# Optimization experiments

Hardware: AMD Instinct MI355X
Metric: run time of the kernel (lower is better)

## Reference

```python
import jax, jax.numpy as jnp
import numpy as np

M = 0.4        # margin
H = 0.333      # margin scaler slope
S = 64.0       # logit scale
BN_MEAN = 20.0     # running_mean of norm normalizer (affine=False, eval stats)
BN_VAR = 100.0 * 100.0
BN_EPS = 1e-3


def setup_inputs() -> dict:
    key = jax.random.key(0)
    k1, k2, k3 = jax.random.split(key, 3)
    embs = jax.random.normal(k1, (1024, 512), dtype=jnp.float32)
    weight = jax.random.normal(k2, (100000, 512), dtype=jnp.float32)
    labels = jax.random.randint(k3, (1024,), 0, 100000)
    return {"embs": embs, "weight": weight, "labels": labels}


def reference(embs, weight, labels):
    n = embs.shape[0]
    rows = jnp.arange(n)
    # feature norms and cosine logits
    norms = jnp.linalg.norm(embs, axis=1, keepdims=True)            # [N,1]
    w_norm = weight / jnp.linalg.norm(weight, axis=1, keepdims=True)  # [C,D]
    logits = (embs / norms) @ w_norm.T                               # [N,C]
    # norm-adaptive margin scaler (BatchNorm1d with running stats, affine=False)
    g = (norms[:, 0] - BN_MEAN) / jnp.sqrt(BN_VAR + BN_EPS)
    g = jnp.clip(g * H, -1.0, 1.0)                                   # [N]
    # angular margin at the label position
    theta = jnp.arccos(jnp.clip(logits.astype(jnp.float32), -0.999, 0.999))
    theta = theta.at[rows, labels].add(-M * g)
    logits_m = jnp.cos(jnp.clip(theta, 0.0, jnp.pi))
    # additive margin at the label position
    logits_m = logits_m.at[rows, labels].add(-(1.0 + M) * g)
    # scaled softmax cross-entropy (mean over batch)
    logp = jax.nn.log_softmax(logits_m * S, axis=-1)
    return -jnp.mean(logp[rows, labels])
```

## Files before the change

kernel.cpp:

```cpp
#include <hip/hip_runtime.h>
#include <math.h>

constexpr int N_ROWS = 1024;
constexpr int DDIM   = 512;
constexpr int C_CLS  = 100000;
constexpr float MARG = 0.4f;
constexpr int NT8    = 784;
constexpr int WPAD8  = 100352;
constexpr int NT_FB  = 782;

typedef __attribute__((ext_vector_type(8))) short bf16x8;
typedef __attribute__((ext_vector_type(4))) float f32x4;
typedef __attribute__((ext_vector_type(4))) int   i32x4;
typedef __attribute__((ext_vector_type(8))) int   i32x8;
typedef __attribute__((address_space(1))) const void gvoid_t;
typedef __attribute__((address_space(3))) void lvoid_t;

__device__ __forceinline__ unsigned int f2bf(float x) {
    union { float f; unsigned int u; } v; v.f = x;
    return (v.u + 0x7FFFu + ((v.u >> 16) & 1u)) >> 16;
}

__device__ __forceinline__ float wave_sum(float s) {
    #pragma unroll
    for (int m = 1; m < 64; m <<= 1) s += __shfl_xor(s, m, 64);
    return s;
}

#if __has_builtin(__builtin_amdgcn_cvt_pk_fp8_f32)
__device__ __forceinline__ unsigned int pk4_e4m3(float a, float b, float c, float d) {
    unsigned int u = (unsigned int)__builtin_amdgcn_cvt_pk_fp8_f32(a, b, 0, false);
    u = (unsigned int)__builtin_amdgcn_cvt_pk_fp8_f32(c, d, (int)u, true);
    return u;
}
#else
__device__ __forceinline__ unsigned int sw_e4m3(float x) {
    x = fminf(fmaxf(x, -448.f), 448.f);
    unsigned int s = (x < 0.f) ? 0x80u : 0u;
    float ax = fabsf(x);
    if (ax < 7.8125e-3f) {
        int q = (int)rintf(ax * 512.f);
        if (q >= 8) return s | 0x08;
        return s | (unsigned int)q;
    }
    int e; float m = frexpf(ax, &e);
    int q = (int)rintf(m * 16.f);
    if (q == 16) { q = 8; e += 1; }
    int E = e - 1 + 7;
    if (E > 15) { E = 15; q = 14; }
    return s | ((unsigned int)E << 3) | (unsigned int)(q - 8);
}
__device__ __forceinline__ unsigned int pk4_e4m3(float a, float b, float c, float d) {
    return sw_e4m3(a) | (sw_e4m3(b) << 8) | (sw_e4m3(c) << 16) | (sw_e4m3(d) << 24);
}
#endif

__device__ __forceinline__ float dec_e4m3(unsigned int b) {
    const unsigned int E = (b >> 3) & 15u, M = b & 7u;
    if (E) {
        union { unsigned int u; float f; } v;
        v.u = ((b & 0x80u) << 24) | ((E + 120u) << 23) | (M << 20);
        return v.f;
    }
    float d = (float)M * 0.001953125f;
    return (b & 0x80u) ? -d : d;
}

__global__ __launch_bounds__(256) void prep_embs8(const float* __restrict__ embs,
                                                  float* __restrict__ g,
                                                  unsigned char* __restrict__ ehat8) {
    const int row  = blockIdx.x * 4 + (threadIdx.x >> 6);
    const int lane = threadIdx.x & 63;
    const float4* src = (const float4*)(embs + (size_t)row * DDIM + lane * 8);
    const float4 a = src[0], b = src[1];
    float ss = a.x*a.x + a.y*a.y + a.z*a.z + a.w*a.w
             + b.x*b.x + b.y*b.y + b.z*b.z + b.w*b.w;
    ss = wave_sum(ss);
    const float norm = sqrtf(ss);
    const float rn = 1.f / norm;
    if (lane == 0) {
        float gg = (norm - 20.f) / sqrtf(10000.f + 1e-3f) * 0.333f;
        gg = fminf(fmaxf(gg, -1.f), 1.f);
        g[row] = gg;
    }
    uint2 pk;
    pk.x = pk4_e4m3(a.x*rn, a.y*rn, a.z*rn, a.w*rn);
    pk.y = pk4_e4m3(b.x*rn, b.y*rn, b.z*rn, b.w*rn);
    *(uint2*)(ehat8 + (size_t)row * DDIM + lane * 8) = pk;
}

__global__ __launch_bounds__(256) void prep_what8(const float* __restrict__ w,
                                                  unsigned char* __restrict__ what8) {
    const int row  = blockIdx.x * 4 + (threadIdx.x >> 6);
    const int lane = threadIdx.x & 63;
    if (row >= C_CLS) {
        *(uint2*)(what8 + (size_t)row * DDIM + lane * 8) = make_uint2(0u, 0u);
        return;
    }
    const float4* src = (const float4*)(w + (size_t)row * DDIM + lane * 8);
    const float4 a = src[0], b = src[1];
    float ss = a.x*a.x + a.y*a.y + a.z*a.z + a.w*a.w
             + b.x*b.x + b.y*b.y + b.z*b.z + b.w*b.w;
    ss = wave_sum(ss);
    const float rn = rsqrtf(ss);
    uint2 pk;
    pk.x = pk4_e4m3(a.x*rn, a.y*rn, a.z*rn, a.w*rn);
    pk.y = pk4_e4m3(b.x*rn, b.y*rn, b.z*rn, b.w*rn);
    *(uint2*)(what8 + (size_t)row * DDIM + lane * 8) = pk;
}

__device__ __forceinline__ i32x8 join8(i32x4 lo, i32x4 hi) {
    return __builtin_shufflevector(lo, hi, 0, 1, 2, 3, 4, 5, 6, 7);
}

__global__ __launch_bounds__(256, 2) void gemm_s1(
        const unsigned char* __restrict__ ehat8,
        const unsigned char* __restrict__ what8,
        float* __restrict__ psum)
{
    __shared__ __align__(16) unsigned char Ab[16384];
    __shared__ __align__(16) unsigned char Bb[16384];
    __shared__ float redbuf[2][128];

    const int tid  = threadIdx.x;
    const int lane = tid & 63;
    const int wv   = tid >> 6;
    const int wr   = wv >> 1;
    const int wc   = wv & 1;
    const int r    = lane & 15;
    const int q    = lane >> 4;

    const int wgid   = ((int)blockIdx.x & 7) * 784 + ((int)blockIdx.x >> 3);
    const int tile_c = wgid >> 3;
    const int tile_r = wgid & 7;
    const int row0   = tile_r * 128;
    const int col0   = tile_c * 128;

    const unsigned char* Asrc = ehat8 + (size_t)(row0 + r) * DDIM + q * 32;
    const unsigned char* Bsrc = what8 + (size_t)(col0 + r) * DDIM + q * 32;

    f32x4 acc[4][4];
    #pragma unroll
    for (int m = 0; m < 4; ++m)
        #pragma unroll
        for (int n = 0; n < 4; ++n) acc[m][n] = f32x4{0.f, 0.f, 0.f, 0.f};

    const int t0 = (int)blockIdx.x & 3;

    for (int it = 0; it < 4; ++it) {
        const int t = (t0 + it) & 3;
        #pragma unroll
        for (int ss = 0; ss < 2; ++ss) {
            const int sl = wv * 2 + ss;
            const unsigned char* ga = Asrc + (size_t)(16 * sl) * DDIM + t * 128;
            __builtin_amdgcn_global_load_lds((gvoid_t*)ga,        (lvoid_t*)(Ab + sl * 2048),        16, 0, 0);
            __builtin_amdgcn_global_load_lds((gvoid_t*)(ga + 16), (lvoid_t*)(Ab + sl * 2048 + 1024), 16, 0, 0);
            const unsigned char* gb = Bsrc + (size_t)(16 * sl) * DDIM + t * 128;
            __builtin_amdgcn_global_load_lds((gvoid_t*)gb,        (lvoid_t*)(Bb + sl * 2048),        16, 0, 0);
            __builtin_amdgcn_global_load_lds((gvoid_t*)(gb + 16), (lvoid_t*)(Bb + sl * 2048 + 1024), 16, 0, 0);
        }
        __syncthreads();

        i32x4 bR[4][2];
        #pragma unroll
        for (int n = 0; n < 4; ++n) {
            bR[n][0] = *(const i32x4*)(Bb + (wc * 4 + n) * 2048 +        lane * 16);
            bR[n][1] = *(const i32x4*)(Bb + (wc * 4 + n) * 2048 + 1024 + lane * 16);
        }
        __builtin_amdgcn_s_setprio(1);
        #pragma unroll
        for (int m = 0; m < 4; ++m) {
            const i32x4 a0 = *(const i32x4*)(Ab + (wr * 4 + m) * 2048 +        lane * 16);
            const i32x4 a1 = *(const i32x4*)(Ab + (wr * 4 + m) * 2048 + 1024 + lane * 16);
            const i32x8 av = join8(a0, a1);
            #pragma unroll
            for (int n = 0; n < 4; ++n)
                acc[m][n] = __builtin_amdgcn_mfma_scale_f32_16x16x128_f8f6f4(
                                av, join8(bR[n][0], bR[n][1]), acc[m][n], 0, 0, 0, 127, 0, 127);
        }
        __builtin_amdgcn_s_setprio(0);
        __syncthreads();
    }

    #pragma unroll
    for (int m = 0; m < 4; ++m) {
        #pragma unroll
        for (int j = 0; j < 4; ++j) {
            const int lrow = wr * 64 + m * 16 + q * 4 + j;
            float s = 0.f;
            #pragma unroll
            for (int n = 0; n < 4; ++n) {
                float v = acc[m][n][j];
                v = fminf(fmaxf(v, -0.999f), 0.999f);
                s += __expf(64.f * v - 64.f);
            }
            #pragma unroll
            for (int msk = 1; msk < 16; msk <<= 1) s += __shfl_xor(s, msk, 64);
            if (r == 0) redbuf[wc][lrow] = s;
        }
    }
    __syncthreads();
    for (int t = tid; t < 128; t += 256)
        psum[(size_t)(row0 + t) * NT8 + tile_c] = redbuf[0][t] + redbuf[1][t];
}

__global__ __launch_bounds__(256) void reduce_rows8(
        const float* __restrict__ psum,
        const unsigned char* __restrict__ ehat8,
        const unsigned char* __restrict__ what8,
        const int* __restrict__ labels,
        const float* __restrict__ g,
        float* __restrict__ losses) {
    const int row  = blockIdx.x * 4 + (threadIdx.x >> 6);
    const int lane = threadIdx.x & 63;
    const float* p = psum + (size_t)row * NT8;
    float s = 0.f;
    for (int t = lane; t < NT8; t += 64) s += p[t];
    const int lab = labels[row];
    const uint2 ea = *(const uint2*)(ehat8 + (size_t)row * DDIM + lane * 8);
    const uint2 wa = *(const uint2*)(what8 + (size_t)lab * DDIM + lane * 8);
    float d = 0.f;
    #pragma unroll
    for (int i = 0; i < 4; ++i)
        d += dec_e4m3((ea.x >> (8 * i)) & 0xFFu) * dec_e4m3((wa.x >> (8 * i)) & 0xFFu);
    #pragma unroll
    for (int i = 0; i < 4; ++i)
        d += dec_e4m3((ea.y >> (8 * i)) & 0xFFu) * dec_e4m3((wa.y >> (8 * i)) & 0xFFu);
    s = wave_sum(s);
    d = wave_sum(d);
    if (lane == 0) {
        const float v  = fminf(fmaxf(d, -0.999f), 0.999f);
        const float gg = g[row];
        float th = acosf(v) - MARG * gg;
        th = fminf(fmaxf(th, 0.f), 3.14159265358979323846f);
        const float vm = cosf(th) - (1.f + MARG) * gg;
        s = s - __expf(64.f * v - 64.f) + __expf(64.f * vm - 64.f);
        losses[row] = 64.f + logf(s) - 64.f * vm;
    }
}

__global__ __launch_bounds__(256) void prep_embs(const float* __restrict__ embs,
                                                 float* __restrict__ g,
                                                 unsigned short* __restrict__ ehat) {
    const int row  = blockIdx.x * 4 + (threadIdx.x >> 6);
    const int lane = threadIdx.x & 63;
    const float4* src = (const float4*)(embs + (size_t)row * DDIM + lane * 8);
    const float4 a = src[0], b = src[1];
    float ss = a.x*a.x + a.y*a.y + a.z*a.z + a.w*a.w
             + b.x*b.x + b.y*b.y + b.z*b.z + b.w*b.w;
    ss = wave_sum(ss);
    const float norm = sqrtf(ss);
    const float rn = 1.f / norm;
    if (lane == 0) {
        float gg = (norm - 20.f) / sqrtf(10000.f + 1e-3f) * 0.333f;
        gg = fminf(fmaxf(gg, -1.f), 1.f);
        g[row] = gg;
    }
    uint4 pk;
    pk.x = f2bf(a.x*rn) | (f2bf(a.y*rn) << 16);
    pk.y = f2bf(a.z*rn) | (f2bf(a.w*rn) << 16);
    pk.z = f2bf(b.x*rn) | (f2bf(b.y*rn) << 16);
    pk.w = f2bf(b.z*rn) | (f2bf(b.w*rn) << 16);
    *(uint4*)(ehat + (size_t)row * DDIM + lane * 8) = pk;
}

__global__ __launch_bounds__(256) void prep_wnorm(const float* __restrict__ w,
                                                  float* __restrict__ rnormw) {
    const int row  = blockIdx.x * 4 + (threadIdx.x >> 6);
    const int lane = threadIdx.x & 63;
    const float4* src = (const float4*)(w + (size_t)row * DDIM + lane * 8);
    const float4 a = src[0], b = src[1];
    float ss = a.x*a.x + a.y*a.y + a.z*a.z + a.w*a.w
             + b.x*b.x + b.y*b.y + b.z*b.z + b.w*b.w;
    ss = wave_sum(ss);
    if (lane == 0) rnormw[row] = 1.f / sqrtf(ss);
}

__global__ __launch_bounds__(256, 2) void gemm_fused_fb(
        const unsigned short* __restrict__ ehat,
        const float* __restrict__ weight,
        const float* __restrict__ rnormw,
        const int* __restrict__ labels,
        float* __restrict__ psum,
        float* __restrict__ dlab)
{
    constexpr int BM = 128, BN = 128, BK = 32;
    __shared__ __align__(16) unsigned short Asf[BM * BK];
    __shared__ __align__(16) unsigned short Bsf[BN * BK];
    __shared__ float redbuf[2][BM];

    const int bid    = blockIdx.x;
    const int tile_c = bid >> 3;
    const int tile_r = bid & 7;
    const int row0   = tile_r * BM;
    const int col0   = tile_c * BN;

    const int tid  = threadIdx.x;
    const int lane = tid & 63;
    const int wv   = tid >> 6;
    const int wr   = wv >> 1;
    const int wc   = wv & 1;

    f32x4 acc[4][4];
    #pragma unroll
    for (int m = 0; m < 4; ++m)
        #pragma unroll
        for (int n = 0; n < 4; ++n) acc[m][n] = f32x4{0.f, 0.f, 0.f, 0.f};

    const int kq    = tid & 7;
    const int brow0 = tid >> 3;
    int   cidx[4];
    float rnv[4];
    #pragma unroll
    for (int p = 0; p < 4; ++p) {
        int c = col0 + p * 32 + brow0;
        c = c < C_CLS ? c : C_CLS - 1;
        cidx[p] = c;
        rnv[p]  = rnormw[c];
    }

    for (int kt = 0; kt < DDIM / BK; ++kt) {
        const int kbase = kt * BK;
        #pragma unroll
        for (int call = 0; call < 2; ++call) {
            const int chunk = call * 256 + tid;
            const uint4 dd = *(const uint4*)(ehat + (size_t)(row0 + (chunk >> 2)) * DDIM
                                             + kbase + (chunk & 3) * 8);
            *(uint4*)(Asf + chunk * 8) = dd;
        }
        #pragma unroll
        for (int p = 0; p < 4; ++p) {
            const float4 wd = *(const float4*)(weight + (size_t)cidx[p] * DDIM + kbase + kq * 4);
            const float rr = rnv[p];
            const unsigned int lo = f2bf(wd.x * rr) | (f2bf(wd.y * rr) << 16);
            const unsigned int hi = f2bf(wd.z * rr) | (f2bf(wd.w * rr) << 16);
            *(uint2*)(Bsf + (p * 32 + brow0) * BK + kq * 4) = make_uint2(lo, hi);
        }
        __syncthreads();
        bf16x8 af[4], bfr[4];
        const int lr  = lane & 15;
        const int lko = (lane >> 4) * 8;
        #pragma unroll
        for (int m = 0; m < 4; ++m)
            af[m] = *(const bf16x8*)(Asf + (wr * 64 + m * 16 + lr) * BK + lko);
        #pragma unroll
        for (int n = 0; n < 4; ++n)
            bfr[n] = *(const bf16x8*)(Bsf + (wc * 64 + n * 16 + lr) * BK + lko);
        #pragma unroll
        for (int m = 0; m < 4; ++m)
            #pragma unroll
            for (int n = 0; n < 4; ++n)
                acc[m][n] = __builtin_amdgcn_mfma_f32_16x16x32_bf16(af[m], bfr[n], acc[m][n], 0, 0, 0);
        __syncthreads();
    }

    #pragma unroll
    for (int m = 0; m < 4; ++m) {
        #pragma unroll
        for (int j = 0; j < 4; ++j) {
            const int lrow  = wr * 64 + m * 16 + ((lane >> 4) << 2) + j;
            const int r_abs = row0 + lrow;
            const int lab   = labels[r_abs];
            float s = 0.f;
            #pragma unroll
            for (int n = 0; n < 4; ++n) {
                const int c_abs = col0 + wc * 64 + n * 16 + (lane & 15);
                float v = acc[m][n][j];
                v = fminf(fmaxf(v, -0.999f), 0.999f);
                if (c_abs == lab) dlab[r_abs] = v;
                if (c_abs < C_CLS) s += __expf(64.f * v - 64.f);
            }
            #pragma unroll
            for (int msk = 1; msk < 16; msk <<= 1) s += __shfl_xor(s, msk, 64);
            if ((lane & 15) == 0) redbuf[wc][lrow] = s;
        }
    }
    __syncthreads();
    for (int t = tid; t < BM; t += 256)
        psum[(size_t)(row0 + t) * NT_FB + tile_c] = redbuf[0][t] + redbuf[1][t];
}

__global__ __launch_bounds__(256) void reduce_rows(const float* __restrict__ psum,
                                                   const float* __restrict__ dlab,
                                                   const float* __restrict__ g,
                                                   float* __restrict__ losses, int nt) {
    const int row  = blockIdx.x * 4 + (threadIdx.x >> 6);
    const int lane = threadIdx.x & 63;
    const float* p = psum + (size_t)row * nt;
    float s = 0.f;
    for (int t = lane; t < nt; t += 64) s += p[t];
    s = wave_sum(s);
    if (lane == 0) {
        const float v  = dlab[row];
        const float gg = g[row];
        float th = acosf(v) - MARG * gg;
        th = fminf(fmaxf(th, 0.f), 3.14159265358979323846f);
        const float vm = cosf(th) - (1.f + MARG) * gg;
        s = s - __expf(64.f * v - 64.f) + __expf(64.f * vm - 64.f);
        losses[row] = 64.f + logf(s) - 64.f * vm;
    }
}

__global__ __launch_bounds__(256) void final_mean(const float* __restrict__ losses,
                                                  float* __restrict__ out) {
    const int tid = threadIdx.x;
    float s = 0.f;
    #pragma unroll
    for (int i = 0; i < 4; ++i) s += losses[tid + i * 256];
    s = wave_sum(s);
    __shared__ float red[4];
    if ((tid & 63) == 0) red[tid >> 6] = s;
    __syncthreads();
    if (tid == 0) out[0] = (red[0] + red[1] + red[2] + red[3]) * (1.f / 1024.f);
}

extern "C" void kernel_launch(void* const* d_in, const int* in_sizes, int n_in,
                              void* d_out, int out_size, void* d_ws, size_t ws_size,
                              hipStream_t stream) {
    const float* embs   = (const float*)d_in[0];
    const float* weight = (const float*)d_in[1];
    const int*   labels = (const int*)d_in[2];
    float* out = (float*)d_out;
    unsigned char* wsb = (unsigned char*)d_ws;

    const size_t WHAT8_B = (size_t)WPAD8 * DDIM;
    const size_t EHAT8_B = (size_t)N_ROWS * DDIM;
    const size_t PSUM_B  = (size_t)N_ROWS * NT8 * 4;
    const size_t NEED_B  = WHAT8_B + EHAT8_B + PSUM_B + 2 * 4096;

    if (ws_size >= NEED_B) {
        unsigned char* what8 = wsb;
        unsigned char* ehat8 = wsb + WHAT8_B;
        float* psum   = (float*)(wsb + WHAT8_B + EHAT8_B);
        float* gbuf   = psum + (size_t)N_ROWS * NT8;
        float* losses = gbuf + 1024;

        prep_embs8<<<N_ROWS / 4, 256, 0, stream>>>(embs, gbuf, ehat8);
        prep_what8<<<WPAD8 / 4, 256, 0, stream>>>(weight, what8);
        gemm_s1<<<NT8 * 8, 256, 0, stream>>>(ehat8, what8, psum);
        reduce_rows8<<<N_ROWS / 4, 256, 0, stream>>>(psum, ehat8, what8, labels, gbuf, losses);
        final_mean<<<1, 256, 0, stream>>>(losses, out);
    } else {
        float* ws = (float*)d_ws;
        float* rnormw = ws + 0;
        float* gbuf   = ws + 100352;
        float* dlab   = ws + 101376;
        float* losses = ws + 102400;
        unsigned short* ehat = (unsigned short*)(ws + 103424);
        float* psum   = ws + 103424 + 262144;

        prep_embs <<<N_ROWS / 4, 256, 0, stream>>>(embs, gbuf, ehat);
        prep_wnorm<<<C_CLS / 4, 256, 0, stream>>>(weight, rnormw);
        gemm_fused_fb<<<NT_FB * 8, 256, 0, stream>>>(ehat, weight, rnormw, labels, psum, dlab);
        reduce_rows<<<N_ROWS / 4, 256, 0, stream>>>(psum, dlab, gbuf, losses, NT_FB);
        final_mean<<<1, 256, 0, stream>>>(losses, out);
    }
}
```

Measured before the change: 183.8 us.

## Fuse weight normalization and FP8 quantization into GEMM, stream all embedding row tiles

The separate prep_what8 pass, which wrote a normalized FP8 copy of the weight matrix to workspace, is removed. Each GEMM workgroup now loads a 64-class panel of fp32 weights, normalizes and quantizes it into LDS, and then streams all eight 128-row embedding tiles through a double-buffered global-to-LDS pipeline, writing one partial exp-sum per row tile. The label-column dot product now uses fp32 weights with its own norm. This removes a full write and reread of the quantized weights and one kernel launch. The costs are heavier LDS use per workgroup, fewer and longer workgroups (1568), and a psum buffer twice as wide.

```diff
diff --git a/kernel.cpp b/kernel.cpp
--- a/kernel.cpp
+++ b/kernel.cpp
@@ -5,8 +5,7 @@
 constexpr int DDIM   = 512;
 constexpr int C_CLS  = 100000;
 constexpr float MARG = 0.4f;
-constexpr int NT8    = 784;
-constexpr int WPAD8  = 100352;
+constexpr int NPAN   = 1568;
 constexpr int NT_FB  = 782;
 
 typedef __attribute__((ext_vector_type(8))) short bf16x8;
@@ -89,37 +88,17 @@
     *(uint2*)(ehat8 + (size_t)row * DDIM + lane * 8) = pk;
 }
 
-__global__ __launch_bounds__(256) void prep_what8(const float* __restrict__ w,
-                                                  unsigned char* __restrict__ what8) {
-    const int row  = blockIdx.x * 4 + (threadIdx.x >> 6);
-    const int lane = threadIdx.x & 63;
-    if (row >= C_CLS) {
-        *(uint2*)(what8 + (size_t)row * DDIM + lane * 8) = make_uint2(0u, 0u);
-        return;
-    }
-    const float4* src = (const float4*)(w + (size_t)row * DDIM + lane * 8);
-    const float4 a = src[0], b = src[1];
-    float ss = a.x*a.x + a.y*a.y + a.z*a.z + a.w*a.w
-             + b.x*b.x + b.y*b.y + b.z*b.z + b.w*b.w;
-    ss = wave_sum(ss);
-    const float rn = rsqrtf(ss);
-    uint2 pk;
-    pk.x = pk4_e4m3(a.x*rn, a.y*rn, a.z*rn, a.w*rn);
-    pk.y = pk4_e4m3(b.x*rn, b.y*rn, b.z*rn, b.w*rn);
-    *(uint2*)(what8 + (size_t)row * DDIM + lane * 8) = pk;
-}
-
 __device__ __forceinline__ i32x8 join8(i32x4 lo, i32x4 hi) {
     return __builtin_shufflevector(lo, hi, 0, 1, 2, 3, 4, 5, 6, 7);
 }
 
-__global__ __launch_bounds__(256, 2) void gemm_s1(
+__global__ __launch_bounds__(256, 2) void gemm_fn(
+        const float* __restrict__ weight,
         const unsigned char* __restrict__ ehat8,
-        const unsigned char* __restrict__ what8,
         float* __restrict__ psum)
 {
-    __shared__ __align__(16) unsigned char Ab[16384];
-    __shared__ __align__(16) unsigned char Bb[16384];
+    __shared__ __align__(16) unsigned char Ab[2][16384];
+    __shared__ __align__(16) unsigned char Bf[32960];
     __shared__ float redbuf[2][128];
 
     const int tid  = threadIdx.x;
@@ -127,109 +106,167 @@
     const int wv   = tid >> 6;
     const int wr   = wv >> 1;
     const int wc   = wv & 1;
-    const int r    = lane & 15;
+    const int r15  = lane & 15;
     const int q    = lane >> 4;
 
-    const int wgid   = ((int)blockIdx.x & 7) * 784 + ((int)blockIdx.x >> 3);
-    const int tile_c = wgid >> 3;
-    const int tile_r = wgid & 7;
-    const int row0   = tile_r * 128;
-    const int col0   = tile_c * 128;
-
-    const unsigned char* Asrc = ehat8 + (size_t)(row0 + r) * DDIM + q * 32;
-    const unsigned char* Bsrc = what8 + (size_t)(col0 + r) * DDIM + q * 32;
-
-    f32x4 acc[4][4];
+    const int wgid = ((int)blockIdx.x & 7) * 196 + ((int)blockIdx.x >> 3);
+    const int col0 = wgid * 64;
+
+    const int j2 = lane >> 2;
+    const int jr = lane & 3;
+    const int tB = lane >> 4;
+    const int qB = j2 & 3;
+    #pragma unroll
+    for (int pass = 0; pass < 4; ++pass) {
+        const int c_rel = wv * 16 + pass * 4 + jr;
+        const int c     = col0 + c_rel;
+        const bool oob  = (c >= C_CLS);
+        const float* wb = weight + (size_t)(oob ? (C_CLS - 1) : c) * DDIM + j2 * 32;
+        float4 v[8];
+        #pragma unroll
+        for (int i = 0; i < 8; ++i) v[i] = ((const float4*)wb)[i];
+        float ss = 0.f;
+        #pragma unroll
+        for (int i = 0; i < 8; ++i)
+            ss += v[i].x*v[i].x + v[i].y*v[i].y + v[i].z*v[i].z + v[i].w*v[i].w;
+        ss += __shfl_xor(ss, 4, 64);  ss += __shfl_xor(ss, 8, 64);
+        ss += __shfl_xor(ss, 16, 64); ss += __shfl_xor(ss, 32, 64);
+        const float sc = oob ? 0.f : rsqrtf(ss);
+        unsigned int u[8];
+        #pragma unroll
+        for (int i = 0; i < 8; ++i)
+            u[i] = pk4_e4m3(v[i].x*sc, v[i].y*sc, v[i].z*sc, v[i].w*sc);
+        unsigned char* wbase = Bf + tB * 8256 + wv * 2048 + (qB * 16 + pass * 4 + jr) * 16;
+        i32x4 lo = {(int)u[0], (int)u[1], (int)u[2], (int)u[3]};
+        i32x4 hi = {(int)u[4], (int)u[5], (int)u[6], (int)u[7]};
+        *(i32x4*)(wbase)        = lo;
+        *(i32x4*)(wbase + 1024) = hi;
+    }
+    asm volatile("s_waitcnt lgkmcnt(0)" ::: "memory");
+    __builtin_amdgcn_sched_barrier(0);
+    __builtin_amdgcn_s_barrier();
+
+    f32x4 acc[4][2];
     #pragma unroll
     for (int m = 0; m < 4; ++m)
         #pragma unroll
-        for (int n = 0; n < 4; ++n) acc[m][n] = f32x4{0.f, 0.f, 0.f, 0.f};
-
-    const int t0 = (int)blockIdx.x & 3;
-
-    for (int it = 0; it < 4; ++it) {
-        const int t = (t0 + it) & 3;
-        #pragma unroll
-        for (int ss = 0; ss < 2; ++ss) {
-            const int sl = wv * 2 + ss;
-            const unsigned char* ga = Asrc + (size_t)(16 * sl) * DDIM + t * 128;
-            __builtin_amdgcn_global_load_lds((gvoid_t*)ga,        (lvoid_t*)(Ab + sl * 2048),        16, 0, 0);
-            __builtin_amdgcn_global_load_lds((gvoid_t*)(ga + 16), (lvoid_t*)(Ab + sl * 2048 + 1024), 16, 0, 0);
-            const unsigned char* gb = Bsrc + (size_t)(16 * sl) * DDIM + t * 128;
-            __builtin_amdgcn_global_load_lds((gvoid_t*)gb,        (lvoid_t*)(Bb + sl * 2048),        16, 0, 0);
-            __builtin_amdgcn_global_load_lds((gvoid_t*)(gb + 16), (lvoid_t*)(Bb + sl * 2048 + 1024), 16, 0, 0);
-        }
-        __syncthreads();
-
-        i32x4 bR[4][2];
-        #pragma unroll
-        for (int n = 0; n < 4; ++n) {
-            bR[n][0] = *(const i32x4*)(Bb + (wc * 4 + n) * 2048 +        lane * 16);
-            bR[n][1] = *(const i32x4*)(Bb + (wc * 4 + n) * 2048 + 1024 + lane * 16);
+        for (int n = 0; n < 2; ++n) acc[m][n] = f32x4{0.f, 0.f, 0.f, 0.f};
+
+#define STAGEA(SLOT, RT, KT) do {                                                   \
+    _Pragma("unroll")                                                               \
+    for (int ss_ = 0; ss_ < 2; ++ss_) {                                             \
+        const int sl_ = wv * 2 + ss_;                                               \
+        const unsigned char* ga_ = ehat8 + (size_t)((RT) * 128 + 16 * sl_ + r15) * DDIM \
+                                   + (KT) * 128 + q * 32;                           \
+        __builtin_amdgcn_global_load_lds((gvoid_t*)ga_,                             \
+            (lvoid_t*)(&Ab[SLOT][sl_ * 2048]), 16, 0, 0);                           \
+        __builtin_amdgcn_global_load_lds((gvoid_t*)(ga_ + 16),                      \
+            (lvoid_t*)(&Ab[SLOT][sl_ * 2048 + 1024]), 16, 0, 0);                    \
+    }                                                                               \
+} while (0)
+
+    STAGEA(0, 0, 0);
+    STAGEA(1, 0, 1);
+
+    for (int p = 0; p < 32; ++p) {
+        const int kt = p & 3, slot = p & 1;
+        if (p == 31) { asm volatile("s_waitcnt vmcnt(0)" ::: "memory"); }
+        else         { asm volatile("s_waitcnt vmcnt(4)" ::: "memory"); }
+        __builtin_amdgcn_s_barrier();
+
+        i32x4 bR[2][2];
+        #pragma unroll
+        for (int n = 0; n < 2; ++n) {
+            bR[n][0] = *(const i32x4*)(Bf + kt * 8256 + (wc * 2 + n) * 2048 +        lane * 16);
+            bR[n][1] = *(const i32x4*)(Bf + kt * 8256 + (wc * 2 + n) * 2048 + 1024 + lane * 16);
+        }
+        i32x4 aR[4][2];
+        #pragma unroll
+        for (int m = 0; m < 4; ++m) {
+            aR[m][0] = *(const i32x4*)(&Ab[slot][(wr * 4 + m) * 2048 +        lane * 16]);
+            aR[m][1] = *(const i32x4*)(&Ab[slot][(wr * 4 + m) * 2048 + 1024 + lane * 16]);
         }
         __builtin_amdgcn_s_setprio(1);
         #pragma unroll
         for (int m = 0; m < 4; ++m) {
-            const i32x4 a0 = *(const i32x4*)(Ab + (wr * 4 + m) * 2048 +        lane * 16);
-            const i32x4 a1 = *(const i32x4*)(Ab + (wr * 4 + m) * 2048 + 1024 + lane * 16);
-            const i32x8 av = join8(a0, a1);
-            #pragma unroll
-            for (int n = 0; n < 4; ++n)
+            const i32x8 av = join8(aR[m][0], aR[m][1]);
+            #pragma unroll
+            for (int n = 0; n < 2; ++n)
                 acc[m][n] = __builtin_amdgcn_mfma_scale_f32_16x16x128_f8f6f4(
                                 av, join8(bR[n][0], bR[n][1]), acc[m][n], 0, 0, 0, 127, 0, 127);
         }
         __builtin_amdgcn_s_setprio(0);
-        __syncthreads();
-    }
-
-    #pragma unroll
-    for (int m = 0; m < 4; ++m) {
-        #pragma unroll
-        for (int j = 0; j < 4; ++j) {
-            const int lrow = wr * 64 + m * 16 + q * 4 + j;
-            float s = 0.f;
-            #pragma unroll
-            for (int n = 0; n < 4; ++n) {
-                float v = acc[m][n][j];
-                v = fminf(fmaxf(v, -0.999f), 0.999f);
-                s += __expf(64.f * v - 64.f);
+        __builtin_amdgcn_s_barrier();
+
+        if (kt == 3) {
+            const int rt = p >> 2;
+            #pragma unroll
+            for (int m = 0; m < 4; ++m) {
+                #pragma unroll
+                for (int j = 0; j < 4; ++j) {
+                    const int lrow = wr * 64 + m * 16 + q * 4 + j;
+                    float s = 0.f;
+                    #pragma unroll
+                    for (int n = 0; n < 2; ++n) {
+                        float v = acc[m][n][j];
+                        v = fminf(fmaxf(v, -0.999f), 0.999f);
+                        s += __expf(64.f * v - 64.f);
+                    }
+                    #pragma unroll
+                    for (int msk = 1; msk < 16; msk <<= 1) s += __shfl_xor(s, msk, 64);
+                    if (r15 == 0) redbuf[wc][lrow] = s;
+                }
             }
-            #pragma unroll
-            for (int msk = 1; msk < 16; msk <<= 1) s += __shfl_xor(s, msk, 64);
-            if (r == 0) redbuf[wc][lrow] = s;
-        }
-    }
-    __syncthreads();
-    for (int t = tid; t < 128; t += 256)
-        psum[(size_t)(row0 + t) * NT8 + tile_c] = redbuf[0][t] + redbuf[1][t];
-}
-
-__global__ __launch_bounds__(256) void reduce_rows8(
+            asm volatile("s_waitcnt lgkmcnt(0)" ::: "memory");
+            __builtin_amdgcn_sched_barrier(0);
+            __builtin_amdgcn_s_barrier();
+            if (tid < 128)
+                psum[(size_t)(rt * 128 + tid) * NPAN + wgid] = redbuf[0][tid] + redbuf[1][tid];
+            __builtin_amdgcn_s_barrier();
+            #pragma unroll
+            for (int m = 0; m < 4; ++m)
+                #pragma unroll
+                for (int n = 0; n < 2; ++n) acc[m][n] = f32x4{0.f, 0.f, 0.f, 0.f};
+        }
+        if (p <= 29) {
+            const int pn = p + 2;
+            STAGEA(pn & 1, pn >> 2, pn & 3);
+        }
+    }
+#undef STAGEA
+}
+
+__global__ __launch_bounds__(256) void reduce_rowsF(
         const float* __restrict__ psum,
         const unsigned char* __restrict__ ehat8,
-        const unsigned char* __restrict__ what8,
+        const float* __restrict__ weight,
         const int* __restrict__ labels,
         const float* __restrict__ g,
         float* __restrict__ losses) {
     const int row  = blockIdx.x * 4 + (threadIdx.x >> 6);
     const int lane = threadIdx.x & 63;
-    const float* p = psum + (size_t)row * NT8;
+    const float* p = psum + (size_t)row * NPAN;
     float s = 0.f;
-    for (int t = lane; t < NT8; t += 64) s += p[t];
+    for (int t = lane; t < NPAN; t += 64) s += p[t];
     const int lab = labels[row];
+    const float4* wv4 = (const float4*)(weight + (size_t)lab * DDIM + lane * 8);
+    const float4 wa = wv4[0], wb = wv4[1];
     const uint2 ea = *(const uint2*)(ehat8 + (size_t)row * DDIM + lane * 8);
-    const uint2 wa = *(const uint2*)(what8 + (size_t)lab * DDIM + lane * 8);
-    float d = 0.f;
-    #pragma unroll
-    for (int i = 0; i < 4; ++i)
-        d += dec_e4m3((ea.x >> (8 * i)) & 0xFFu) * dec_e4m3((wa.x >> (8 * i)) & 0xFFu);
-    #pragma unroll
-    for (int i = 0; i < 4; ++i)
-        d += dec_e4m3((ea.y >> (8 * i)) & 0xFFu) * dec_e4m3((wa.y >> (8 * i)) & 0xFFu);
-    s = wave_sum(s);
-    d = wave_sum(d);
+    float wsq = wa.x*wa.x + wa.y*wa.y + wa.z*wa.z + wa.w*wa.w
+              + wb.x*wb.x + wb.y*wb.y + wb.z*wb.z + wb.w*wb.w;
+    float d = dec_e4m3( ea.x        & 0xFFu) * wa.x
+            + dec_e4m3((ea.x >>  8) & 0xFFu) * wa.y
+            + dec_e4m3((ea.x >> 16) & 0xFFu) * wa.z
+            + dec_e4m3((ea.x >> 24) & 0xFFu) * wa.w
+            + dec_e4m3( ea.y        & 0xFFu) * wb.x
+            + dec_e4m3((ea.y >>  8) & 0xFFu) * wb.y
+            + dec_e4m3((ea.y >> 16) & 0xFFu) * wb.z
+            + dec_e4m3((ea.y >> 24) & 0xFFu) * wb.w;
+    s   = wave_sum(s);
+    d   = wave_sum(d);
+    wsq = wave_sum(wsq);
     if (lane == 0) {
-        const float v  = fminf(fmaxf(d, -0.999f), 0.999f);
+        const float v  = fminf(fmaxf(d * rsqrtf(wsq), -0.999f), 0.999f);
         const float gg = g[row];
         float th = acosf(v) - MARG * gg;
         th = fminf(fmaxf(th, 0.f), 3.14159265358979323846f);
@@ -423,22 +460,19 @@
     float* out = (float*)d_out;
     unsigned char* wsb = (unsigned char*)d_ws;
 
-    const size_t WHAT8_B = (size_t)WPAD8 * DDIM;
     const size_t EHAT8_B = (size_t)N_ROWS * DDIM;
-    const size_t PSUM_B  = (size_t)N_ROWS * NT8 * 4;
-    const size_t NEED_B  = WHAT8_B + EHAT8_B + PSUM_B + 2 * 4096;
+    const size_t PSUM_B  = (size_t)N_ROWS * NPAN * 4;
+    const size_t NEED_B  = EHAT8_B + PSUM_B + 2 * 4096;
 
     if (ws_size >= NEED_B) {
-        unsigned char* what8 = wsb;
-        unsigned char* ehat8 = wsb + WHAT8_B;
-        float* psum   = (float*)(wsb + WHAT8_B + EHAT8_B);
-        float* gbuf   = psum + (size_t)N_ROWS * NT8;
+        unsigned char* ehat8 = wsb;
+        float* psum   = (float*)(wsb + EHAT8_B);
+        float* gbuf   = (float*)(wsb + EHAT8_B + PSUM_B);
         float* losses = gbuf + 1024;
 
         prep_embs8<<<N_ROWS / 4, 256, 0, stream>>>(embs, gbuf, ehat8);
-        prep_what8<<<WPAD8 / 4, 256, 0, stream>>>(weight, what8);
-        gemm_s1<<<NT8 * 8, 256, 0, stream>>>(ehat8, what8, psum);
-        reduce_rows8<<<N_ROWS / 4, 256, 0, stream>>>(psum, ehat8, what8, labels, gbuf, losses);
+        gemm_fn<<<NPAN, 256, 0, stream>>>(weight, ehat8, psum);
+        reduce_rowsF<<<N_ROWS / 4, 256, 0, stream>>>(psum, ehat8, weight, labels, gbuf, losses);
         final_mean<<<1, 256, 0, stream>>>(losses, out);
     } else {
         float* ws = (float*)d_ws;
```

After: 264.7 us. +44.0%, slower.

## Stage full A tile in LDS and stream B directly into registers with double buffering

Applied to the files above, without the earlier changes.

The GEMM kernel now loads the entire 128x512 FP8 A tile into 64 KB of LDS up front. B fragments are read straight from global memory into registers, alternating between two register sets so the next load overlaps the current MFMA phase, with explicit vmcnt waits. This removes the per-K-step LDS staging and two __syncthreads per iteration for B. In exchange it uses much more LDS, which may drop occupancy below two blocks per CU, and the hand-counted waitcnt scheduling is fragile.

```diff
diff --git a/kernel.cpp b/kernel.cpp
--- a/kernel.cpp
+++ b/kernel.cpp
@@ -15,6 +15,8 @@
 typedef __attribute__((ext_vector_type(8))) int   i32x8;
 typedef __attribute__((address_space(1))) const void gvoid_t;
 typedef __attribute__((address_space(3))) void lvoid_t;
+
+#define WAITV(N) asm volatile("s_waitcnt vmcnt(" #N ")" ::: "memory")
 
 __device__ __forceinline__ unsigned int f2bf(float x) {
     union { float f; unsigned int u; } v; v.f = x;
@@ -113,13 +115,12 @@
     return __builtin_shufflevector(lo, hi, 0, 1, 2, 3, 4, 5, 6, 7);
 }
 
-__global__ __launch_bounds__(256, 2) void gemm_s1(
+__global__ __launch_bounds__(256, 2) void gemm_bd(
         const unsigned char* __restrict__ ehat8,
         const unsigned char* __restrict__ what8,
         float* __restrict__ psum)
 {
-    __shared__ __align__(16) unsigned char Ab[16384];
-    __shared__ __align__(16) unsigned char Bb[16384];
+    __shared__ __align__(16) unsigned char Ab[65536];
     __shared__ float redbuf[2][128];
 
     const int tid  = threadIdx.x;
@@ -127,7 +128,7 @@
     const int wv   = tid >> 6;
     const int wr   = wv >> 1;
     const int wc   = wv & 1;
-    const int r    = lane & 15;
+    const int r15  = lane & 15;
     const int q    = lane >> 4;
 
     const int wgid   = ((int)blockIdx.x & 7) * 784 + ((int)blockIdx.x >> 3);
@@ -136,51 +137,72 @@
     const int row0   = tile_r * 128;
     const int col0   = tile_c * 128;
 
-    const unsigned char* Asrc = ehat8 + (size_t)(row0 + r) * DDIM + q * 32;
-    const unsigned char* Bsrc = what8 + (size_t)(col0 + r) * DDIM + q * 32;
-
-    f32x4 acc[4][4];
-    #pragma unroll
-    for (int m = 0; m < 4; ++m)
-        #pragma unroll
-        for (int n = 0; n < 4; ++n) acc[m][n] = f32x4{0.f, 0.f, 0.f, 0.f};
-
-    const int t0 = (int)blockIdx.x & 3;
-
-    for (int it = 0; it < 4; ++it) {
-        const int t = (t0 + it) & 3;
+    #pragma unroll
+    for (int t = 0; t < 4; ++t) {
         #pragma unroll
         for (int ss = 0; ss < 2; ++ss) {
             const int sl = wv * 2 + ss;
-            const unsigned char* ga = Asrc + (size_t)(16 * sl) * DDIM + t * 128;
-            __builtin_amdgcn_global_load_lds((gvoid_t*)ga,        (lvoid_t*)(Ab + sl * 2048),        16, 0, 0);
-            __builtin_amdgcn_global_load_lds((gvoid_t*)(ga + 16), (lvoid_t*)(Ab + sl * 2048 + 1024), 16, 0, 0);
-            const unsigned char* gb = Bsrc + (size_t)(16 * sl) * DDIM + t * 128;
-            __builtin_amdgcn_global_load_lds((gvoid_t*)gb,        (lvoid_t*)(Bb + sl * 2048),        16, 0, 0);
-            __builtin_amdgcn_global_load_lds((gvoid_t*)(gb + 16), (lvoid_t*)(Bb + sl * 2048 + 1024), 16, 0, 0);
+            const unsigned char* ga = ehat8 + (size_t)(row0 + 16 * sl + r15) * DDIM
+                                      + t * 128 + q * 32;
+            __builtin_amdgcn_global_load_lds((gvoid_t*)ga,
+                (lvoid_t*)(Ab + t * 16384 + sl * 2048), 16, 0, 0);
+            __builtin_amdgcn_global_load_lds((gvoid_t*)(ga + 16),
+                (lvoid_t*)(Ab + t * 16384 + sl * 2048 + 1024), 16, 0, 0);
         }
-        __syncthreads();
-
-        i32x4 bR[4][2];
-        #pragma unroll
-        for (int n = 0; n < 4; ++n) {
-            bR[n][0] = *(const i32x4*)(Bb + (wc * 4 + n) * 2048 +        lane * 16);
-            bR[n][1] = *(const i32x4*)(Bb + (wc * 4 + n) * 2048 + 1024 + lane * 16);
-        }
-        __builtin_amdgcn_s_setprio(1);
-        #pragma unroll
-        for (int m = 0; m < 4; ++m) {
-            const i32x4 a0 = *(const i32x4*)(Ab + (wr * 4 + m) * 2048 +        lane * 16);
-            const i32x4 a1 = *(const i32x4*)(Ab + (wr * 4 + m) * 2048 + 1024 + lane * 16);
-            const i32x8 av = join8(a0, a1);
-            #pragma unroll
-            for (int n = 0; n < 4; ++n)
-                acc[m][n] = __builtin_amdgcn_mfma_scale_f32_16x16x128_f8f6f4(
-                                av, join8(bR[n][0], bR[n][1]), acc[m][n], 0, 0, 0, 127, 0, 127);
-        }
-        __builtin_amdgcn_s_setprio(0);
-        __syncthreads();
-    }
+    }
+
+    const unsigned char* Bsrc = what8 + (size_t)(col0 + r15) * DDIM + q * 32;
+    i32x4 S0[2][2], S1[2][2];
+
+#define LDB(S, T, U) do {                                                        \
+    _Pragma("unroll")                                                            \
+    for (int n = 0; n < 2; ++n)                                                  \
+        _Pragma("unroll")                                                        \
+        for (int h = 0; h < 2; ++h)                                              \
+            S[n][h] = *(const i32x4*)(Bsrc                                       \
+                + (size_t)((wc * 4 + (U) * 2 + n) * 16) * DDIM                   \
+                + (T) * 128 + h * 16);                                           \
+} while (0)
+
+#define PH(T, U, S) do {                                                         \
+    __builtin_amdgcn_s_setprio(1);                                               \
+    _Pragma("unroll")                                                            \
+    for (int m = 0; m < 4; ++m) {                                                \
+        const i32x4 a0 = *(const i32x4*)(Ab + (T) * 16384 + (wr * 4 + m) * 2048  \
+                                         + lane * 16);                           \
+        const i32x4 a1 = *(const i32x4*)(Ab + (T) * 16384 + (wr * 4 + m) * 2048  \
+                                         + 1024 + lane * 16);                    \
+        const i32x8 av = join8(a0, a1);                                          \
+        _Pragma("unroll")                                                        \
+        for (int n = 0; n < 2; ++n)                                              \
+            acc[m][(U) * 2 + n] = __builtin_amdgcn_mfma_scale_f32_16x16x128_f8f6f4( \
+                av, join8(S[n][0], S[n][1]), acc[m][(U) * 2 + n], 0, 0, 0, 127, 0, 127); \
+    }                                                                            \
+    __builtin_amdgcn_s_setprio(0);                                               \
+} while (0)
+
+    LDB(S0, 0, 0);
+    LDB(S1, 0, 1);
+
+    f32x4 acc[4][4];
+    #pragma unroll
+    for (int m = 0; m < 4; ++m)
+        #pragma unroll
+        for (int n = 0; n < 4; ++n) acc[m][n] = f32x4{0.f, 0.f, 0.f, 0.f};
+
+    asm volatile("s_waitcnt vmcnt(8)" ::: "memory");
+    __builtin_amdgcn_s_barrier();
+
+    WAITV(4); PH(0, 0, S0); LDB(S0, 1, 0);
+    WAITV(4); PH(0, 1, S1); LDB(S1, 1, 1);
+    WAITV(4); PH(1, 0, S0); LDB(S0, 2, 0);
+    WAITV(4); PH(1, 1, S1); LDB(S1, 2, 1);
+    WAITV(4); PH(2, 0, S0); LDB(S0, 3, 0);
+    WAITV(4); PH(2, 1, S1); LDB(S1, 3, 1);
+    WAITV(4); PH(3, 0, S0);
+    WAITV(0); PH(3, 1, S1);
+#undef LDB
+#undef PH
 
     #pragma unroll
     for (int m = 0; m < 4; ++m) {
@@ -196,7 +218,7 @@
             }
             #pragma unroll
             for (int msk = 1; msk < 16; msk <<= 1) s += __shfl_xor(s, msk, 64);
-            if (r == 0) redbuf[wc][lrow] = s;
+            if (r15 == 0) redbuf[wc][lrow] = s;
         }
     }
     __syncthreads();
@@ -437,7 +459,7 @@
 
         prep_embs8<<<N_ROWS / 4, 256, 0, stream>>>(embs, gbuf, ehat8);
         prep_what8<<<WPAD8 / 4, 256, 0, stream>>>(weight, what8);
-        gemm_s1<<<NT8 * 8, 256, 0, stream>>>(ehat8, what8, psum);
+        gemm_bd<<<NT8 * 8, 256, 0, stream>>>(ehat8, what8, psum);
         reduce_rows8<<<N_ROWS / 4, 256, 0, stream>>>(psum, ehat8, what8, labels, gbuf, losses);
         final_mean<<<1, 256, 0, stream>>>(losses, out);
     } else {
```

After: 324.7 us. 76.7% more time.

## Double-buffer LDS tiles in FP8 GEMM to overlap global loads with MFMA

Applied to the files above, without the earlier changes.

Turns the single-buffered LDS staging in the FP8 cosine GEMM into a double-buffered pipeline. The first two K-slices are prefetched, each step reads its A and B fragments into registers, and the load of slice t+2 is issued into the freed buffer before the MFMAs run. Explicit vmcnt/lgkmcnt waits and raw s_barrier replace __syncthreads. The aim is to hide global-to-LDS latency behind compute. In exchange LDS use doubles to about 64KB per block, which may limit occupancy, and the staggered K-start order per block is dropped.

```diff
diff --git a/kernel.cpp b/kernel.cpp
--- a/kernel.cpp
+++ b/kernel.cpp
@@ -15,6 +15,8 @@
 typedef __attribute__((ext_vector_type(8))) int   i32x8;
 typedef __attribute__((address_space(1))) const void gvoid_t;
 typedef __attribute__((address_space(3))) void lvoid_t;
+
+#define WAITV(N) asm volatile("s_waitcnt vmcnt(" #N ")" ::: "memory")
 
 __device__ __forceinline__ unsigned int f2bf(float x) {
     union { float f; unsigned int u; } v; v.f = x;
@@ -113,13 +115,13 @@
     return __builtin_shufflevector(lo, hi, 0, 1, 2, 3, 4, 5, 6, 7);
 }
 
-__global__ __launch_bounds__(256, 2) void gemm_s1(
+__global__ __launch_bounds__(256, 2) void gemm_db(
         const unsigned char* __restrict__ ehat8,
         const unsigned char* __restrict__ what8,
         float* __restrict__ psum)
 {
-    __shared__ __align__(16) unsigned char Ab[16384];
-    __shared__ __align__(16) unsigned char Bb[16384];
+    __shared__ __align__(16) unsigned char Ab[2][16384];
+    __shared__ __align__(16) unsigned char Bb[2][16384];
     __shared__ float redbuf[2][128];
 
     const int tid  = threadIdx.x;
@@ -127,7 +129,7 @@
     const int wv   = tid >> 6;
     const int wr   = wv >> 1;
     const int wc   = wv & 1;
-    const int r    = lane & 15;
+    const int r15  = lane & 15;
     const int q    = lane >> 4;
 
     const int wgid   = ((int)blockIdx.x & 7) * 784 + ((int)blockIdx.x >> 3);
@@ -136,8 +138,25 @@
     const int row0   = tile_r * 128;
     const int col0   = tile_c * 128;
 
-    const unsigned char* Asrc = ehat8 + (size_t)(row0 + r) * DDIM + q * 32;
-    const unsigned char* Bsrc = what8 + (size_t)(col0 + r) * DDIM + q * 32;
+    const unsigned char* Asrc = ehat8 + (size_t)(row0 + r15) * DDIM + q * 32;
+    const unsigned char* Bsrc = what8 + (size_t)(col0 + r15) * DDIM + q * 32;
+
+#define STAGE(BUF, T) do {                                                       \
+    _Pragma("unroll")                                                            \
+    for (int ss_ = 0; ss_ < 2; ++ss_) {                                          \
+        const int sl_ = wv * 2 + ss_;                                            \
+        const unsigned char* ga_ = Asrc + (size_t)(16 * sl_) * DDIM + (T) * 128; \
+        __builtin_amdgcn_global_load_lds((gvoid_t*)ga_,                          \
+            (lvoid_t*)(&Ab[BUF][sl_ * 2048]), 16, 0, 0);                         \
+        __builtin_amdgcn_global_load_lds((gvoid_t*)(ga_ + 16),                   \
+            (lvoid_t*)(&Ab[BUF][sl_ * 2048 + 1024]), 16, 0, 0);                  \
+        const unsigned char* gb_ = Bsrc + (size_t)(16 * sl_) * DDIM + (T) * 128; \
+        __builtin_amdgcn_global_load_lds((gvoid_t*)gb_,                          \
+            (lvoid_t*)(&Bb[BUF][sl_ * 2048]), 16, 0, 0);                         \
+        __builtin_amdgcn_global_load_lds((gvoid_t*)(gb_ + 16),                   \
+            (lvoid_t*)(&Bb[BUF][sl_ * 2048 + 1024]), 16, 0, 0);                  \
+    }                                                                            \
+} while (0)
 
     f32x4 acc[4][4];
     #pragma unroll
@@ -145,42 +164,44 @@
         #pragma unroll
         for (int n = 0; n < 4; ++n) acc[m][n] = f32x4{0.f, 0.f, 0.f, 0.f};
 
-    const int t0 = (int)blockIdx.x & 3;
-
-    for (int it = 0; it < 4; ++it) {
-        const int t = (t0 + it) & 3;
-        #pragma unroll
-        for (int ss = 0; ss < 2; ++ss) {
-            const int sl = wv * 2 + ss;
-            const unsigned char* ga = Asrc + (size_t)(16 * sl) * DDIM + t * 128;
-            __builtin_amdgcn_global_load_lds((gvoid_t*)ga,        (lvoid_t*)(Ab + sl * 2048),        16, 0, 0);
-            __builtin_amdgcn_global_load_lds((gvoid_t*)(ga + 16), (lvoid_t*)(Ab + sl * 2048 + 1024), 16, 0, 0);
-            const unsigned char* gb = Bsrc + (size_t)(16 * sl) * DDIM + t * 128;
-            __builtin_amdgcn_global_load_lds((gvoid_t*)gb,        (lvoid_t*)(Bb + sl * 2048),        16, 0, 0);
-            __builtin_amdgcn_global_load_lds((gvoid_t*)(gb + 16), (lvoid_t*)(Bb + sl * 2048 + 1024), 16, 0, 0);
-        }
-        __syncthreads();
-
-        i32x4 bR[4][2];
+    STAGE(0, 0);
+    STAGE(1, 1);
+    WAITV(8);
+    __builtin_amdgcn_s_barrier();
+
+    #pragma unroll
+    for (int t = 0; t < 4; ++t) {
+        const int buf = t & 1;
+        i32x4 aR[4][2], bR[4][2];
         #pragma unroll
         for (int n = 0; n < 4; ++n) {
-            bR[n][0] = *(const i32x4*)(Bb + (wc * 4 + n) * 2048 +        lane * 16);
-            bR[n][1] = *(const i32x4*)(Bb + (wc * 4 + n) * 2048 + 1024 + lane * 16);
-        }
+            bR[n][0] = *(const i32x4*)(&Bb[buf][(wc * 4 + n) * 2048 +        lane * 16]);
+            bR[n][1] = *(const i32x4*)(&Bb[buf][(wc * 4 + n) * 2048 + 1024 + lane * 16]);
+        }
+        #pragma unroll
+        for (int m = 0; m < 4; ++m) {
+            aR[m][0] = *(const i32x4*)(&Ab[buf][(wr * 4 + m) * 2048 +        lane * 16]);
+            aR[m][1] = *(const i32x4*)(&Ab[buf][(wr * 4 + m) * 2048 + 1024 + lane * 16]);
+        }
+        asm volatile("s_waitcnt lgkmcnt(0)" ::: "memory");
+        __builtin_amdgcn_sched_barrier(0);
+        __builtin_amdgcn_s_barrier();
+        if (t < 2) STAGE(buf, t + 2);
         __builtin_amdgcn_s_setprio(1);
         #pragma unroll
         for (int m = 0; m < 4; ++m) {
-            const i32x4 a0 = *(const i32x4*)(Ab + (wr * 4 + m) * 2048 +        lane * 16);
-            const i32x4 a1 = *(const i32x4*)(Ab + (wr * 4 + m) * 2048 + 1024 + lane * 16);
-            const i32x8 av = join8(a0, a1);
+            const i32x8 av = join8(aR[m][0], aR[m][1]);
             #pragma unroll
             for (int n = 0; n < 4; ++n)
                 acc[m][n] = __builtin_amdgcn_mfma_scale_f32_16x16x128_f8f6f4(
                                 av, join8(bR[n][0], bR[n][1]), acc[m][n], 0, 0, 0, 127, 0, 127);
         }
         __builtin_amdgcn_s_setprio(0);
-        __syncthreads();
-    }
+        if (t < 2)      { WAITV(8); }
+        else if (t == 2){ WAITV(0); }
+        if (t < 3) __builtin_amdgcn_s_barrier();
+    }
+#undef STAGE
 
     #pragma unroll
     for (int m = 0; m < 4; ++m) {
@@ -196,7 +217,7 @@
             }
             #pragma unroll
             for (int msk = 1; msk < 16; msk <<= 1) s += __shfl_xor(s, msk, 64);
-            if (r == 0) redbuf[wc][lrow] = s;
+            if (r15 == 0) redbuf[wc][lrow] = s;
         }
     }
     __syncthreads();
@@ -437,7 +458,7 @@
 
         prep_embs8<<<N_ROWS / 4, 256, 0, stream>>>(embs, gbuf, ehat8);
         prep_what8<<<WPAD8 / 4, 256, 0, stream>>>(weight, what8);
-        gemm_s1<<<NT8 * 8, 256, 0, stream>>>(ehat8, what8, psum);
+        gemm_db<<<NT8 * 8, 256, 0, stream>>>(ehat8, what8, psum);
         reduce_rows8<<<N_ROWS / 4, 256, 0, stream>>>(psum, ehat8, what8, labels, gbuf, losses);
         final_mean<<<1, 256, 0, stream>>>(losses, out);
     } else {
```

Result: no change. 186.9 us (+1.7%).
